# Optimization experiments

Measured on AMD Instinct MI355X. Metric: run time of the kernel, lower is better.

Reference implementation:

```python
import jax, jax.numpy as jnp
import numpy as np

NUM_LAYERS = 3
CHANNELS = 8
IN_CHANNELS = 8
MASK_OUT_STRIDE = 4


def resize_align_corners(x, oh, ow):
    # Bilinear resize with align_corners=True, x: [N, C, H, W]
    n, c, h, w = x.shape
    ys = jnp.linspace(0.0, h - 1.0, oh)
    xs = jnp.linspace(0.0, w - 1.0, ow)
    y0 = jnp.clip(jnp.floor(ys).astype(jnp.int32), 0, h - 2)
    x0 = jnp.clip(jnp.floor(xs).astype(jnp.int32), 0, w - 2)
    wy = (ys - y0.astype(ys.dtype)).astype(x.dtype)[None, None, :, None]
    wx = (xs - x0.astype(xs.dtype)).astype(x.dtype)[None, None, None, :]
    top = x[:, :, y0, :]
    bot = x[:, :, y0 + 1, :]
    row = top * (1.0 - wy) + bot * wy          # [n,c,oh,w]
    left = row[:, :, :, x0]
    right = row[:, :, :, x0 + 1]
    return left * (1.0 - wx) + right * wx       # [n,c,oh,ow]


def aligned_bilinear(t, factor):
    # Faithful port of adet.utils.comm.aligned_bilinear
    if factor == 1:
        return t
    h, w = t.shape[2], t.shape[3]
    t = jnp.pad(t, ((0, 0), (0, 0), (0, 1), (0, 1)), mode="edge")
    oh, ow = factor * h + 1, factor * w + 1
    t = resize_align_corners(t, oh, ow)
    p = factor // 2
    t = jnp.pad(t, ((0, 0), (0, 0), (p, 0), (p, 0)), mode="edge")
    return t[:, :, : oh - 1, : ow - 1]


def reference(mask_feats, mask_head_params, locations_inst, soi, im_inds, fpn_levels, mask_feat_stride):
    N, C, H, W = mask_feats.shape
    n_inst = mask_head_params.shape[0]
    # compute_locations at mask_feat_stride (x fastest, matching torch meshgrid order)
    half = mask_feat_stride // 2
    sx = jnp.arange(W, dtype=mask_feats.dtype) * mask_feat_stride + half
    sy = jnp.arange(H, dtype=mask_feats.dtype) * mask_feat_stride + half
    gy, gx = jnp.meshgrid(sy, sx, indexing="ij")
    locs = jnp.stack([gx.reshape(-1), gy.reshape(-1)], axis=1)  # [HW, 2]
    # relative coords, normalized by size-of-interest of instance's FPN level
    rel = locations_inst[:, None, :] - locs[None, :, :]          # [n, HW, 2]
    rel = jnp.transpose(rel, (0, 2, 1))                          # [n, 2, HW]
    rel = rel / soi[fpn_levels][:, None, None]
    feats = mask_feats[im_inds].reshape(n_inst, IN_CHANNELS, H * W)
    x = jnp.concatenate([rel.astype(mask_feats.dtype), feats], axis=1)  # [n, 10, HW]
    # parse_dynamic_params: split flat params into per-instance weights/biases
    wn = [(IN_CHANNELS + 2) * CHANNELS, CHANNELS * CHANNELS, CHANNELS * 1]
    bn = [CHANNELS, CHANNELS, 1]
    offs = np.cumsum([0] + wn + bn)
    parts = [mask_head_params[:, offs[i]:offs[i + 1]] for i in range(6)]
    w0 = parts[0].reshape(n_inst, CHANNELS, IN_CHANNELS + 2)
    w1 = parts[1].reshape(n_inst, CHANNELS, CHANNELS)
    w2 = parts[2].reshape(n_inst, 1, CHANNELS)
    b0, b1, b2 = parts[3], parts[4], parts[5]
    # per-instance dynamic MLP (1x1 grouped conv == batched matmul)
    x = jax.nn.relu(jnp.einsum("noi,nip->nop", w0, x) + b0[:, :, None])
    x = jax.nn.relu(jnp.einsum("noi,nip->nop", w1, x) + b1[:, :, None])
    x = jnp.einsum("noi,nip->nop", w2, x) + b2[:, :, None]
    logits = x.reshape(n_inst, 1, H, W)
    factor = int(mask_feat_stride // MASK_OUT_STRIDE)
    return aligned_bilinear(logits, factor)


def setup_inputs() -> dict:
    key = jax.random.key(0)
    k0, k1, k2, k3, k4 = jax.random.split(key, 5)
    N, C, H, W = 4, IN_CHANNELS, 128, 192
    n_inst = 128
    stride = 8
    num_gen_params = (IN_CHANNELS + 2) * CHANNELS + CHANNELS * CHANNELS + CHANNELS + CHANNELS + CHANNELS + 1  # 169
    mask_feats = jax.random.normal(k0, (N, C, H, W), dtype=jnp.float32)
    mask_head_params = jax.random.normal(k1, (n_inst, num_gen_params), dtype=jnp.float32) * 0.1
    locations_inst = jax.random.uniform(k2, (n_inst, 2), dtype=jnp.float32) * jnp.array([W * stride, H * stride], jnp.float32)
    soi = jnp.array([64.0, 128.0, 256.0, 512.0, 1024.0], jnp.float32)
    im_inds = jax.random.randint(k3, (n_inst,), 0, N)
    fpn_levels = jax.random.randint(k4, (n_inst,), 0, 5)
    return {
        "mask_feats": mask_feats,
        "mask_head_params": mask_head_params,
        "locations_inst": locations_inst,
        "soi": soi,
        "im_inds": im_inds,
        "fpn_levels": fpn_levels,
        "mask_feat_stride": stride,
    }
```

## Files before the change

### kernel.cpp

```cpp
#include <hip/hip_runtime.h>

#define HH 128
#define WW 192
#define HW (HH * WW)

typedef float f32x4 __attribute__((ext_vector_type(4)));
typedef __fp16 h2 __attribute__((ext_vector_type(2)));

__device__ __forceinline__ float relu(float v) { return fmaxf(v, 0.0f); }

__device__ __forceinline__ float fdot2(h2 a, h2 b, float c) {
#if __has_builtin(__builtin_amdgcn_fdot2)
    return __builtin_amdgcn_fdot2(a, b, c, false);
#else
    return fmaf((float)a.x, (float)b.x, fmaf((float)a.y, (float)b.y, c));
#endif
}
__device__ __forceinline__ h2 pkrtz(float a, float b) {
    return __builtin_amdgcn_cvt_pkrtz(a, b);
}


__global__ __launch_bounds__(512) void dmh_kernel(
    const float* __restrict__ mask_feats,
    const float* __restrict__ params,
    const float* __restrict__ locs,
    const float* __restrict__ soi,
    const int*   __restrict__ im_inds,
    const int*   __restrict__ fpn_levels,
    const int*   __restrict__ stride_p,
    float*       __restrict__ out)
{
    const int tid = threadIdx.x;
    const int c0 = blockIdx.x * 64;
    const int r0 = blockIdx.y * 32;
    const int n  = blockIdx.z;

    __shared__ h2    sWp[68];
    __shared__ float sF[33];
    __shared__ float tile[33 * 66];

    if (tid < 169) {
        float v = params[(size_t)n * 169 + tid];
        __fp16* sWh = reinterpret_cast<__fp16*>(sWp);
        if (tid < 80) {
            int o = tid / 10, k = tid - o * 10;
            if (k == 0)      sF[o] = v;
            else if (k == 1) sF[8 + o] = v;
            else { int f = k - 2; sWh[(o * 4 + (f >> 1)) * 2 + (f & 1)] = (__fp16)v; }
        } else if (tid < 144) {
            int t = tid - 80, o = t >> 3, i = t & 7;
            sWh[(32 + o * 4 + (i >> 1)) * 2 + (i & 1)] = (__fp16)v;
        } else if (tid < 152) {
            int o = tid - 144;
            sWh[(64 + (o >> 1)) * 2 + (o & 1)] = (__fp16)v;
        } else if (tid < 160) sF[16 + (tid - 152)] = v;
        else if (tid < 168)   sF[24 + (tid - 160)] = v;
        else                  sF[32] = v;
    }

    const int   stride = *stride_p;
    const float half_s = 0.5f * (float)stride;
    const float locx = locs[2 * n + 0];
    const float locy = locs[2 * n + 1];
    const float inv  = 1.0f / soi[fpn_levels[n]];
    const float* fb  = mask_feats + (size_t)im_inds[n] * 8 * HW;

    const int ir = tid >> 4;
    const int ic = (tid & 15) << 2;
    const int rr = r0 + ir, cc = c0 + ic;
    const float* fp = fb + rr * WW + cc;

    f32x4 xv[8];
    #pragma unroll
    for (int ch = 0; ch < 8; ++ch)
        xv[ch] = *reinterpret_cast<const f32x4*>(fp + ch * HW);

    __syncthreads();

    {
        const float rxd = -(float)stride * inv;
        float rx[4];
        rx[0] = (locx - (float)(cc * stride) - half_s) * inv;
        rx[1] = rx[0] + rxd; rx[2] = rx[1] + rxd; rx[3] = rx[2] + rxd;
        const float ry = (locy - (float)(rr * stride) - half_s) * inv;

        h2 xp[4][4];
        #pragma unroll
        for (int p = 0; p < 4; ++p)
            #pragma unroll
            for (int j = 0; j < 4; ++j)
                xp[p][j] = pkrtz(xv[2 * p][j], xv[2 * p + 1][j]);

        float h[8][4];
        #pragma unroll
        for (int o = 0; o < 8; ++o) {
            const h2 w0 = sWp[o * 4 + 0], w1 = sWp[o * 4 + 1],
                     w2 = sWp[o * 4 + 2], w3 = sWp[o * 4 + 3];
            float tO = fmaf(sF[8 + o], ry, sF[16 + o]);
            float wx = sF[o];
            #pragma unroll
            for (int j = 0; j < 4; ++j) {
                float acc = fmaf(wx, rx[j], tO);
                acc = fdot2(w0, xp[0][j], acc);
                acc = fdot2(w1, xp[1][j], acc);
                acc = fdot2(w2, xp[2][j], acc);
                acc = fdot2(w3, xp[3][j], acc);
                h[o][j] = acc;
            }
        }

        h2 hp[4][4];
        #pragma unroll
        for (int p = 0; p < 4; ++p)
            #pragma unroll
            for (int j = 0; j < 4; ++j)
                hp[p][j] = pkrtz(relu(h[2 * p][j]), relu(h[2 * p + 1][j]));

        float a[8][4];
        #pragma unroll
        for (int o = 0; o < 8; ++o) {
            const h2 w0 = sWp[32 + o * 4 + 0], w1 = sWp[32 + o * 4 + 1],
                     w2 = sWp[32 + o * 4 + 2], w3 = sWp[32 + o * 4 + 3];
            float b1 = sF[24 + o];
            #pragma unroll
            for (int j = 0; j < 4; ++j) {
                float acc = b1;
                acc = fdot2(w0, hp[0][j], acc);
                acc = fdot2(w1, hp[1][j], acc);
                acc = fdot2(w2, hp[2][j], acc);
                acc = fdot2(w3, hp[3][j], acc);
                a[o][j] = acc;
            }
        }

        const h2 v0 = sWp[64], v1 = sWp[65], v2 = sWp[66], v3 = sWp[67];
        const float b2v = sF[32];
        #pragma unroll
        for (int j = 0; j < 4; ++j) {
            h2 a0 = pkrtz(relu(a[0][j]), relu(a[1][j]));
            h2 a1 = pkrtz(relu(a[2][j]), relu(a[3][j]));
            h2 a2 = pkrtz(relu(a[4][j]), relu(a[5][j]));
            h2 a3 = pkrtz(relu(a[6][j]), relu(a[7][j]));
            float lg = b2v;
            lg = fdot2(v0, a0, lg);
            lg = fdot2(v1, a1, lg);
            lg = fdot2(v2, a2, lg);
            lg = fdot2(v3, a3, lg);
            tile[(ir + 1) * 66 + ic + 1 + j] = lg;
        }
    }

    if (tid < 97) {
        int r, c;
        if (tid < 65) { r = -1; c = tid - 1; }
        else          { r = tid - 65; c = -1; }
        int hr = min(max(r0 + r, 0), HH - 1);
        int hc = min(max(c0 + c, 0), WW - 1);
        const float* hfp = fb + hr * WW + hc;
        float rx  = (locx - (float)(hc * stride) - half_s) * inv;
        float ry2 = (locy - (float)(hr * stride) - half_s) * inv;
        h2 xp[4];
        #pragma unroll
        for (int p = 0; p < 4; ++p)
            xp[p] = pkrtz(hfp[(2 * p) * HW], hfp[(2 * p + 1) * HW]);
        float hh[8];
        #pragma unroll
        for (int o = 0; o < 8; ++o) {
            float acc = fmaf(sF[o], rx, fmaf(sF[8 + o], ry2, sF[16 + o]));
            #pragma unroll
            for (int p = 0; p < 4; ++p) acc = fdot2(sWp[o * 4 + p], xp[p], acc);
            hh[o] = acc;
        }
        h2 hp[4];
        #pragma unroll
        for (int p = 0; p < 4; ++p)
            hp[p] = pkrtz(relu(hh[2 * p]), relu(hh[2 * p + 1]));
        float aa[8];
        #pragma unroll
        for (int o = 0; o < 8; ++o) {
            float acc = sF[24 + o];
            #pragma unroll
            for (int p = 0; p < 4; ++p) acc = fdot2(sWp[32 + o * 4 + p], hp[p], acc);
            aa[o] = acc;
        }
        float lg = sF[32];
        #pragma unroll
        for (int p = 0; p < 4; ++p) {
            h2 ap = pkrtz(relu(aa[2 * p]), relu(aa[2 * p + 1]));
            lg = fdot2(sWp[64 + p], ap, lg);
        }
        tile[(r + 1) * 66 + (c + 1)] = lg;
    }
    __syncthreads();

    const int kx = tid & 31;
    const int ky = tid >> 5;
    float* ob = out + ((size_t)n * 256 + 2 * r0) * 384 + 2 * c0 + 4 * kx;
    #pragma unroll
    for (int yy = 0; yy < 4; ++yy) {
        int yt = ky * 4 + yy;
        int iy = yt - 1;
        int rbl = iy >> 1;
        int fy = iy & 1;
        float wy0 = fy ? 0.5f : 1.0f;
        float wy1 = fy ? 0.5f : 0.0f;
        int sr  = rbl + 1;
        int sr2 = sr + fy;
        const float* ra = &tile[sr  * 66 + 2 * kx];
        const float* rc = &tile[sr2 * 66 + 2 * kx];
        float t0 = fmaf(wy1, rc[0], wy0 * ra[0]);
        float t1 = fmaf(wy1, rc[1], wy0 * ra[1]);
        float t2 = fmaf(wy1, rc[2], wy0 * ra[2]);
        f32x4 o4;
        o4.x = 0.5f * (t0 + t1);
        o4.y = t1;
        o4.z = 0.5f * (t1 + t2);
        o4.w = t2;
        __builtin_nontemporal_store(o4, reinterpret_cast<f32x4*>(ob + (size_t)yt * 384));
    }
}

extern "C" void kernel_launch(void* const* d_in, const int* in_sizes, int n_in,
                              void* d_out, int out_size, void* d_ws, size_t ws_size,
                              hipStream_t stream) {
    const float* mask_feats = (const float*)d_in[0];
    const float* params     = (const float*)d_in[1];
    const float* locs       = (const float*)d_in[2];
    const float* soi        = (const float*)d_in[3];
    const int*   im_inds    = (const int*)d_in[4];
    const int*   fpn_levels = (const int*)d_in[5];
    const int*   stride_p   = (const int*)d_in[6];
    float* out = (float*)d_out;

    dim3 grid(WW / 64, HH / 32, 128);
    dim3 block(512);
    dmh_kernel<<<grid, block, 0, stream>>>(
        mask_feats, params, locs, soi, im_inds, fpn_levels, stride_p, out);
}
```

Measured before the change: 20.44 us.

## Map one wavefront per row pair and upsample in registers via lane shuffles

Each wavefront now owns two input rows across the full 192-column width, with each lane handling three columns. The next row's logits are recomputed locally, and horizontal neighbours come from a cross-lane shuffle instead of a shared-memory tile. This drops the LDS tile, the separate halo computation and the second barrier, and the bilinear upsample is done entirely in registers. The cost is about 50% recomputation of the MLP on the overlapping row, scalar three-element loads that are not 16-byte aligned, and narrower 8-byte stores.

After: 27.82 us. 36.1% more time.

```diff
diff --git a/kernel.cpp b/kernel.cpp
--- a/kernel.cpp
+++ b/kernel.cpp
@@ -4,24 +4,19 @@
 #define WW 192
 #define HW (HH * WW)
 
-typedef float f32x4 __attribute__((ext_vector_type(4)));
+typedef float f32x2v __attribute__((ext_vector_type(2)));
 typedef __fp16 h2 __attribute__((ext_vector_type(2)));
 
 __device__ __forceinline__ float relu(float v) { return fmaxf(v, 0.0f); }
-
 __device__ __forceinline__ float fdot2(h2 a, h2 b, float c) {
-#if __has_builtin(__builtin_amdgcn_fdot2)
     return __builtin_amdgcn_fdot2(a, b, c, false);
-#else
-    return fmaf((float)a.x, (float)b.x, fmaf((float)a.y, (float)b.y, c));
-#endif
 }
 __device__ __forceinline__ h2 pkrtz(float a, float b) {
     return __builtin_amdgcn_cvt_pkrtz(a, b);
 }
 
 
-__global__ __launch_bounds__(512) void dmh_kernel(
+__global__ __launch_bounds__(256) void dmh_kernel(
     const float* __restrict__ mask_feats,
     const float* __restrict__ params,
     const float* __restrict__ locs,
@@ -31,14 +26,15 @@
     const int*   __restrict__ stride_p,
     float*       __restrict__ out)
 {
-    const int tid = threadIdx.x;
-    const int c0 = blockIdx.x * 64;
-    const int r0 = blockIdx.y * 32;
-    const int n  = blockIdx.z;
+    const int tid  = threadIdx.x;
+    const int lane = tid & 63;
+    const int wid  = tid >> 6;
+    const int g    = blockIdx.x * 4 + wid;
+    const int r    = 2 * g;
+    const int n    = blockIdx.y;
 
     __shared__ h2    sWp[68];
     __shared__ float sF[33];
-    __shared__ float tile[33 * 66];
 
     if (tid < 169) {
         float v = params[(size_t)n * 169 + tid];
@@ -66,42 +62,46 @@
     const float inv  = 1.0f / soi[fpn_levels[n]];
     const float* fb  = mask_feats + (size_t)im_inds[n] * 8 * HW;
 
-    const int ir = tid >> 4;
-    const int ic = (tid & 15) << 2;
-    const int rr = r0 + ir, cc = c0 + ic;
-    const float* fp = fb + rr * WW + cc;
-
-    f32x4 xv[8];
+    __syncthreads();
+
+    const int col0 = 3 * lane;
+    const float rxd = -(float)stride * inv;
+    float rx0 = (locx - (float)(col0 * stride) - half_s) * inv;
+    float rx1 = rx0 + rxd;
+    float rx2 = rx1 + rxd;
+
+    float L[3][3];
     #pragma unroll
-    for (int ch = 0; ch < 8; ++ch)
-        xv[ch] = *reinterpret_cast<const f32x4*>(fp + ch * HW);
-
-    __syncthreads();
-
-    {
-        const float rxd = -(float)stride * inv;
-        float rx[4];
-        rx[0] = (locx - (float)(cc * stride) - half_s) * inv;
-        rx[1] = rx[0] + rxd; rx[2] = rx[1] + rxd; rx[3] = rx[2] + rxd;
-        const float ry = (locy - (float)(rr * stride) - half_s) * inv;
-
-        h2 xp[4][4];
+    for (int i = 0; i < 3; ++i) {
+        const int srow = min(r + i, HH - 1);
+        const float* fp = fb + srow * WW + col0;
+        const float ry = (locy - (float)(srow * stride) - half_s) * inv;
+
+        float x[8][3];
+        #pragma unroll
+        for (int ch = 0; ch < 8; ++ch) {
+            x[ch][0] = fp[ch * HW + 0];
+            x[ch][1] = fp[ch * HW + 1];
+            x[ch][2] = fp[ch * HW + 2];
+        }
+        h2 xp[4][3];
         #pragma unroll
         for (int p = 0; p < 4; ++p)
             #pragma unroll
-            for (int j = 0; j < 4; ++j)
-                xp[p][j] = pkrtz(xv[2 * p][j], xv[2 * p + 1][j]);
-
-        float h[8][4];
+            for (int j = 0; j < 3; ++j)
+                xp[p][j] = pkrtz(x[2 * p][j], x[2 * p + 1][j]);
+
+        float h[8][3];
         #pragma unroll
         for (int o = 0; o < 8; ++o) {
             const h2 w0 = sWp[o * 4 + 0], w1 = sWp[o * 4 + 1],
                      w2 = sWp[o * 4 + 2], w3 = sWp[o * 4 + 3];
             float tO = fmaf(sF[8 + o], ry, sF[16 + o]);
             float wx = sF[o];
-            #pragma unroll
-            for (int j = 0; j < 4; ++j) {
-                float acc = fmaf(wx, rx[j], tO);
+            float rxj[3] = {rx0, rx1, rx2};
+            #pragma unroll
+            for (int j = 0; j < 3; ++j) {
+                float acc = fmaf(wx, rxj[j], tO);
                 acc = fdot2(w0, xp[0][j], acc);
                 acc = fdot2(w1, xp[1][j], acc);
                 acc = fdot2(w2, xp[2][j], acc);
@@ -109,22 +109,21 @@
                 h[o][j] = acc;
             }
         }
-
-        h2 hp[4][4];
+        h2 hp[4][3];
         #pragma unroll
         for (int p = 0; p < 4; ++p)
             #pragma unroll
-            for (int j = 0; j < 4; ++j)
+            for (int j = 0; j < 3; ++j)
                 hp[p][j] = pkrtz(relu(h[2 * p][j]), relu(h[2 * p + 1][j]));
 
-        float a[8][4];
+        float a[8][3];
         #pragma unroll
         for (int o = 0; o < 8; ++o) {
             const h2 w0 = sWp[32 + o * 4 + 0], w1 = sWp[32 + o * 4 + 1],
                      w2 = sWp[32 + o * 4 + 2], w3 = sWp[32 + o * 4 + 3];
             float b1 = sF[24 + o];
             #pragma unroll
-            for (int j = 0; j < 4; ++j) {
+            for (int j = 0; j < 3; ++j) {
                 float acc = b1;
                 acc = fdot2(w0, hp[0][j], acc);
                 acc = fdot2(w1, hp[1][j], acc);
@@ -133,11 +132,10 @@
                 a[o][j] = acc;
             }
         }
-
         const h2 v0 = sWp[64], v1 = sWp[65], v2 = sWp[66], v3 = sWp[67];
         const float b2v = sF[32];
         #pragma unroll
-        for (int j = 0; j < 4; ++j) {
+        for (int j = 0; j < 3; ++j) {
             h2 a0 = pkrtz(relu(a[0][j]), relu(a[1][j]));
             h2 a1 = pkrtz(relu(a[2][j]), relu(a[3][j]));
             h2 a2 = pkrtz(relu(a[4][j]), relu(a[5][j]));
@@ -147,78 +145,42 @@
             lg = fdot2(v1, a1, lg);
             lg = fdot2(v2, a2, lg);
             lg = fdot2(v3, a3, lg);
-            tile[(ir + 1) * 66 + ic + 1 + j] = lg;
-        }
-    }
-
-    if (tid < 97) {
-        int r, c;
-        if (tid < 65) { r = -1; c = tid - 1; }
-        else          { r = tid - 65; c = -1; }
-        int hr = min(max(r0 + r, 0), HH - 1);
-        int hc = min(max(c0 + c, 0), WW - 1);
-        const float* hfp = fb + hr * WW + hc;
-        float rx  = (locx - (float)(hc * stride) - half_s) * inv;
-        float ry2 = (locy - (float)(hr * stride) - half_s) * inv;
-        h2 xp[4];
-        #pragma unroll
-        for (int p = 0; p < 4; ++p)
-            xp[p] = pkrtz(hfp[(2 * p) * HW], hfp[(2 * p + 1) * HW]);
-        float hh[8];
-        #pragma unroll
-        for (int o = 0; o < 8; ++o) {
-            float acc = fmaf(sF[o], rx, fmaf(sF[8 + o], ry2, sF[16 + o]));
-            #pragma unroll
-            for (int p = 0; p < 4; ++p) acc = fdot2(sWp[o * 4 + p], xp[p], acc);
-            hh[o] = acc;
-        }
-        h2 hp[4];
-        #pragma unroll
-        for (int p = 0; p < 4; ++p)
-            hp[p] = pkrtz(relu(hh[2 * p]), relu(hh[2 * p + 1]));
-        float aa[8];
-        #pragma unroll
-        for (int o = 0; o < 8; ++o) {
-            float acc = sF[24 + o];
-            #pragma unroll
-            for (int p = 0; p < 4; ++p) acc = fdot2(sWp[32 + o * 4 + p], hp[p], acc);
-            aa[o] = acc;
-        }
-        float lg = sF[32];
-        #pragma unroll
-        for (int p = 0; p < 4; ++p) {
-            h2 ap = pkrtz(relu(aa[2 * p]), relu(aa[2 * p + 1]));
-            lg = fdot2(sWp[64 + p], ap, lg);
-        }
-        tile[(r + 1) * 66 + (c + 1)] = lg;
-    }
-    __syncthreads();
-
-    const int kx = tid & 31;
-    const int ky = tid >> 5;
-    float* ob = out + ((size_t)n * 256 + 2 * r0) * 384 + 2 * c0 + 4 * kx;
+            L[i][j] = lg;
+        }
+    }
+
+    float ci[3][6];
     #pragma unroll
-    for (int yy = 0; yy < 4; ++yy) {
-        int yt = ky * 4 + yy;
-        int iy = yt - 1;
-        int rbl = iy >> 1;
-        int fy = iy & 1;
-        float wy0 = fy ? 0.5f : 1.0f;
-        float wy1 = fy ? 0.5f : 0.0f;
-        int sr  = rbl + 1;
-        int sr2 = sr + fy;
-        const float* ra = &tile[sr  * 66 + 2 * kx];
-        const float* rc = &tile[sr2 * 66 + 2 * kx];
-        float t0 = fmaf(wy1, rc[0], wy0 * ra[0]);
-        float t1 = fmaf(wy1, rc[1], wy0 * ra[1]);
-        float t2 = fmaf(wy1, rc[2], wy0 * ra[2]);
-        f32x4 o4;
-        o4.x = 0.5f * (t0 + t1);
-        o4.y = t1;
-        o4.z = 0.5f * (t1 + t2);
-        o4.w = t2;
-        __builtin_nontemporal_store(o4, reinterpret_cast<f32x4*>(ob + (size_t)yt * 384));
-    }
+    for (int i = 0; i < 3; ++i) {
+        float Lm1 = __shfl_up(L[i][2], 1);
+        if (lane == 0) Lm1 = L[i][0];
+        ci[i][0] = 0.5f * (Lm1 + L[i][0]);
+        ci[i][1] = L[i][0];
+        ci[i][2] = 0.5f * (L[i][0] + L[i][1]);
+        ci[i][3] = L[i][1];
+        ci[i][4] = 0.5f * (L[i][1] + L[i][2]);
+        ci[i][5] = L[i][2];
+    }
+
+    float* ob = out + (size_t)n * 256 * 384 + 6 * lane;
+    auto store_row = [&](int y, const float* v) {
+        float* p = ob + (size_t)y * 384;
+        f32x2v s0 = {v[0], v[1]}, s1 = {v[2], v[3]}, s2 = {v[4], v[5]};
+        *reinterpret_cast<f32x2v*>(p + 0) = s0;
+        *reinterpret_cast<f32x2v*>(p + 2) = s1;
+        *reinterpret_cast<f32x2v*>(p + 4) = s2;
+    };
+    float mid1[6], mid2[6];
+    #pragma unroll
+    for (int k = 0; k < 6; ++k) {
+        mid1[k] = 0.5f * (ci[0][k] + ci[1][k]);
+        mid2[k] = 0.5f * (ci[1][k] + ci[2][k]);
+    }
+    if (g == 0) store_row(0, ci[0]);
+    store_row(2 * r + 1, ci[0]);
+    store_row(2 * r + 2, mid1);
+    store_row(2 * r + 3, ci[1]);
+    if (2 * r + 4 <= 255) store_row(2 * r + 4, mid2);
 }
 
 extern "C" void kernel_launch(void* const* d_in, const int* in_sizes, int n_in,
@@ -233,8 +195,8 @@
     const int*   stride_p   = (const int*)d_in[6];
     float* out = (float*)d_out;
 
-    dim3 grid(WW / 64, HH / 32, 128);
-    dim3 block(512);
+    dim3 grid(16, 128);
+    dim3 block(256);
     dmh_kernel<<<grid, block, 0, stream>>>(
         mask_feats, params, locs, soi, im_inds, fpn_levels, stride_p, out);
 }
```

## Split fused kernel into logits pass and separate upsample pass via workspace

Applied to the files above, without the earlier changes.

Replaces the single fused kernel, which computed the MLP logits for a tile plus a recomputed halo and then upsampled from shared memory, with two kernels. The first writes full-resolution logits to a global workspace without halo recomputation. The second reads them back and does the 2x aligned bilinear upsample. This removes the redundant halo MLP work and the intra-block syncs, but adds a global round trip of the logits and a second launch.

Result: slower. 32.29 us (+58.0%).

```diff
diff --git a/kernel.cpp b/kernel.cpp
--- a/kernel.cpp
+++ b/kernel.cpp
@@ -3,25 +3,21 @@
 #define HH 128
 #define WW 192
 #define HW (HH * WW)
+#define PXI (HH * WW)
 
 typedef float f32x4 __attribute__((ext_vector_type(4)));
 typedef __fp16 h2 __attribute__((ext_vector_type(2)));
 
 __device__ __forceinline__ float relu(float v) { return fmaxf(v, 0.0f); }
-
 __device__ __forceinline__ float fdot2(h2 a, h2 b, float c) {
-#if __has_builtin(__builtin_amdgcn_fdot2)
     return __builtin_amdgcn_fdot2(a, b, c, false);
-#else
-    return fmaf((float)a.x, (float)b.x, fmaf((float)a.y, (float)b.y, c));
-#endif
 }
 __device__ __forceinline__ h2 pkrtz(float a, float b) {
     return __builtin_amdgcn_cvt_pkrtz(a, b);
 }
 
 
-__global__ __launch_bounds__(512) void dmh_kernel(
+__global__ __launch_bounds__(512) void logits_kernel(
     const float* __restrict__ mask_feats,
     const float* __restrict__ params,
     const float* __restrict__ locs,
@@ -29,16 +25,14 @@
     const int*   __restrict__ im_inds,
     const int*   __restrict__ fpn_levels,
     const int*   __restrict__ stride_p,
-    float*       __restrict__ out)
+    float*       __restrict__ ws)
 {
     const int tid = threadIdx.x;
-    const int c0 = blockIdx.x * 64;
-    const int r0 = blockIdx.y * 32;
-    const int n  = blockIdx.z;
+    const int bx  = blockIdx.x;
+    const int n   = blockIdx.y;
 
     __shared__ h2    sWp[68];
     __shared__ float sF[33];
-    __shared__ float tile[33 * 66];
 
     if (tid < 169) {
         float v = params[(size_t)n * 169 + tid];
@@ -66,10 +60,10 @@
     const float inv  = 1.0f / soi[fpn_levels[n]];
     const float* fb  = mask_feats + (size_t)im_inds[n] * 8 * HW;
 
-    const int ir = tid >> 4;
-    const int ic = (tid & 15) << 2;
-    const int rr = r0 + ir, cc = c0 + ic;
-    const float* fp = fb + rr * WW + cc;
+    const int px  = bx * 2048 + tid * 4;
+    const int row = px / WW;
+    const int col = px - row * WW;
+    const float* fp = fb + px;
 
     f32x4 xv[8];
     #pragma unroll
@@ -78,146 +72,117 @@
 
     __syncthreads();
 
-    {
-        const float rxd = -(float)stride * inv;
-        float rx[4];
-        rx[0] = (locx - (float)(cc * stride) - half_s) * inv;
-        rx[1] = rx[0] + rxd; rx[2] = rx[1] + rxd; rx[3] = rx[2] + rxd;
-        const float ry = (locy - (float)(rr * stride) - half_s) * inv;
-
-        h2 xp[4][4];
-        #pragma unroll
-        for (int p = 0; p < 4; ++p)
-            #pragma unroll
-            for (int j = 0; j < 4; ++j)
-                xp[p][j] = pkrtz(xv[2 * p][j], xv[2 * p + 1][j]);
-
-        float h[8][4];
-        #pragma unroll
-        for (int o = 0; o < 8; ++o) {
-            const h2 w0 = sWp[o * 4 + 0], w1 = sWp[o * 4 + 1],
-                     w2 = sWp[o * 4 + 2], w3 = sWp[o * 4 + 3];
-            float tO = fmaf(sF[8 + o], ry, sF[16 + o]);
-            float wx = sF[o];
-            #pragma unroll
-            for (int j = 0; j < 4; ++j) {
-                float acc = fmaf(wx, rx[j], tO);
-                acc = fdot2(w0, xp[0][j], acc);
-                acc = fdot2(w1, xp[1][j], acc);
-                acc = fdot2(w2, xp[2][j], acc);
-                acc = fdot2(w3, xp[3][j], acc);
-                h[o][j] = acc;
-            }
+    const float rxd = -(float)stride * inv;
+    float rx[4];
+    rx[0] = (locx - (float)(col * stride) - half_s) * inv;
+    rx[1] = rx[0] + rxd; rx[2] = rx[1] + rxd; rx[3] = rx[2] + rxd;
+    const float ry = (locy - (float)(row * stride) - half_s) * inv;
+
+    h2 xp[4][4];
+    #pragma unroll
+    for (int p = 0; p < 4; ++p)
+        #pragma unroll
+        for (int j = 0; j < 4; ++j)
+            xp[p][j] = pkrtz(xv[2 * p][j], xv[2 * p + 1][j]);
+
+    float h[8][4];
+    #pragma unroll
+    for (int o = 0; o < 8; ++o) {
+        const h2 w0 = sWp[o * 4 + 0], w1 = sWp[o * 4 + 1],
+                 w2 = sWp[o * 4 + 2], w3 = sWp[o * 4 + 3];
+        float tO = fmaf(sF[8 + o], ry, sF[16 + o]);
+        float wx = sF[o];
+        #pragma unroll
+        for (int j = 0; j < 4; ++j) {
+            float acc = fmaf(wx, rx[j], tO);
+            acc = fdot2(w0, xp[0][j], acc);
+            acc = fdot2(w1, xp[1][j], acc);
+            acc = fdot2(w2, xp[2][j], acc);
+            acc = fdot2(w3, xp[3][j], acc);
+            h[o][j] = acc;
         }
-
-        h2 hp[4][4];
-        #pragma unroll
-        for (int p = 0; p < 4; ++p)
-            #pragma unroll
-            for (int j = 0; j < 4; ++j)
-                hp[p][j] = pkrtz(relu(h[2 * p][j]), relu(h[2 * p + 1][j]));
-
-        float a[8][4];
-        #pragma unroll
-        for (int o = 0; o < 8; ++o) {
-            const h2 w0 = sWp[32 + o * 4 + 0], w1 = sWp[32 + o * 4 + 1],
-                     w2 = sWp[32 + o * 4 + 2], w3 = sWp[32 + o * 4 + 3];
-            float b1 = sF[24 + o];
-            #pragma unroll
-            for (int j = 0; j < 4; ++j) {
-                float acc = b1;
-                acc = fdot2(w0, hp[0][j], acc);
-                acc = fdot2(w1, hp[1][j], acc);
-                acc = fdot2(w2, hp[2][j], acc);
-                acc = fdot2(w3, hp[3][j], acc);
-                a[o][j] = acc;
-            }
+    }
+    h2 hp[4][4];
+    #pragma unroll
+    for (int p = 0; p < 4; ++p)
+        #pragma unroll
+        for (int j = 0; j < 4; ++j)
+            hp[p][j] = pkrtz(relu(h[2 * p][j]), relu(h[2 * p + 1][j]));
+
+    float a[8][4];
+    #pragma unroll
+    for (int o = 0; o < 8; ++o) {
+        const h2 w0 = sWp[32 + o * 4 + 0], w1 = sWp[32 + o * 4 + 1],
+                 w2 = sWp[32 + o * 4 + 2], w3 = sWp[32 + o * 4 + 3];
+        float b1 = sF[24 + o];
+        #pragma unroll
+        for (int j = 0; j < 4; ++j) {
+            float acc = b1;
+            acc = fdot2(w0, hp[0][j], acc);
+            acc = fdot2(w1, hp[1][j], acc);
+            acc = fdot2(w2, hp[2][j], acc);
+            acc = fdot2(w3, hp[3][j], acc);
+            a[o][j] = acc;
         }
-
-        const h2 v0 = sWp[64], v1 = sWp[65], v2 = sWp[66], v3 = sWp[67];
-        const float b2v = sF[32];
-        #pragma unroll
-        for (int j = 0; j < 4; ++j) {
-            h2 a0 = pkrtz(relu(a[0][j]), relu(a[1][j]));
-            h2 a1 = pkrtz(relu(a[2][j]), relu(a[3][j]));
-            h2 a2 = pkrtz(relu(a[4][j]), relu(a[5][j]));
-            h2 a3 = pkrtz(relu(a[6][j]), relu(a[7][j]));
-            float lg = b2v;
-            lg = fdot2(v0, a0, lg);
-            lg = fdot2(v1, a1, lg);
-            lg = fdot2(v2, a2, lg);
-            lg = fdot2(v3, a3, lg);
-            tile[(ir + 1) * 66 + ic + 1 + j] = lg;
-        }
-    }
-
-    if (tid < 97) {
-        int r, c;
-        if (tid < 65) { r = -1; c = tid - 1; }
-        else          { r = tid - 65; c = -1; }
-        int hr = min(max(r0 + r, 0), HH - 1);
-        int hc = min(max(c0 + c, 0), WW - 1);
-        const float* hfp = fb + hr * WW + hc;
-        float rx  = (locx - (float)(hc * stride) - half_s) * inv;
-        float ry2 = (locy - (float)(hr * stride) - half_s) * inv;
-        h2 xp[4];
-        #pragma unroll
-        for (int p = 0; p < 4; ++p)
-            xp[p] = pkrtz(hfp[(2 * p) * HW], hfp[(2 * p + 1) * HW]);
-        float hh[8];
-        #pragma unroll
-        for (int o = 0; o < 8; ++o) {
-            float acc = fmaf(sF[o], rx, fmaf(sF[8 + o], ry2, sF[16 + o]));
-            #pragma unroll
-            for (int p = 0; p < 4; ++p) acc = fdot2(sWp[o * 4 + p], xp[p], acc);
-            hh[o] = acc;
-        }
-        h2 hp[4];
-        #pragma unroll
-        for (int p = 0; p < 4; ++p)
-            hp[p] = pkrtz(relu(hh[2 * p]), relu(hh[2 * p + 1]));
-        float aa[8];
-        #pragma unroll
-        for (int o = 0; o < 8; ++o) {
-            float acc = sF[24 + o];
-            #pragma unroll
-            for (int p = 0; p < 4; ++p) acc = fdot2(sWp[32 + o * 4 + p], hp[p], acc);
-            aa[o] = acc;
-        }
-        float lg = sF[32];
-        #pragma unroll
-        for (int p = 0; p < 4; ++p) {
-            h2 ap = pkrtz(relu(aa[2 * p]), relu(aa[2 * p + 1]));
-            lg = fdot2(sWp[64 + p], ap, lg);
-        }
-        tile[(r + 1) * 66 + (c + 1)] = lg;
-    }
-    __syncthreads();
-
-    const int kx = tid & 31;
-    const int ky = tid >> 5;
-    float* ob = out + ((size_t)n * 256 + 2 * r0) * 384 + 2 * c0 + 4 * kx;
-    #pragma unroll
-    for (int yy = 0; yy < 4; ++yy) {
-        int yt = ky * 4 + yy;
-        int iy = yt - 1;
-        int rbl = iy >> 1;
-        int fy = iy & 1;
-        float wy0 = fy ? 0.5f : 1.0f;
-        float wy1 = fy ? 0.5f : 0.0f;
-        int sr  = rbl + 1;
-        int sr2 = sr + fy;
-        const float* ra = &tile[sr  * 66 + 2 * kx];
-        const float* rc = &tile[sr2 * 66 + 2 * kx];
-        float t0 = fmaf(wy1, rc[0], wy0 * ra[0]);
-        float t1 = fmaf(wy1, rc[1], wy0 * ra[1]);
-        float t2 = fmaf(wy1, rc[2], wy0 * ra[2]);
+    }
+    const h2 v0 = sWp[64], v1 = sWp[65], v2 = sWp[66], v3 = sWp[67];
+    const float b2v = sF[32];
+    f32x4 lg;
+    #pragma unroll
+    for (int j = 0; j < 4; ++j) {
+        h2 a0 = pkrtz(relu(a[0][j]), relu(a[1][j]));
+        h2 a1 = pkrtz(relu(a[2][j]), relu(a[3][j]));
+        h2 a2 = pkrtz(relu(a[4][j]), relu(a[5][j]));
+        h2 a3 = pkrtz(relu(a[6][j]), relu(a[7][j]));
+        float l = b2v;
+        l = fdot2(v0, a0, l);
+        l = fdot2(v1, a1, l);
+        l = fdot2(v2, a2, l);
+        l = fdot2(v3, a3, l);
+        lg[j] = l;
+    }
+    *reinterpret_cast<f32x4*>(ws + (size_t)n * PXI + px) = lg;
+}
+
+__global__ __launch_bounds__(256) void upsample_kernel(
+    const float* __restrict__ ws,
+    float*       __restrict__ out)
+{
+    const int tid = threadIdx.x;
+    const int g0  = blockIdx.x * 1024 + tid;
+
+    #pragma unroll
+    for (int k = 0; k < 4; ++k) {
+        const int g   = g0 + k * 256;
+        const int yg  = g / 96;
+        const int f4c = g - yg * 96;
+        const int n   = yg >> 8;
+        const int y   = yg & 255;
+
+        const int iy = y - 1;
+        const int rb = iy >> 1;
+        const int fy = iy & 1;
+        const float wy0 = fy ? 0.5f : 1.0f;
+        const float wy1 = fy ? 0.5f : 0.0f;
+        const int r1 = max(rb, 0);
+        const int r2 = rb + fy;
+
+        const float* La = ws + (size_t)n * PXI + r1 * WW;
+        const float* Lb = ws + (size_t)n * PXI + r2 * WW;
+
+        const int m0 = 2 * f4c - 1;
+        const int mc = max(m0, 0);
+        float t0 = fmaf(wy1, Lb[mc],     wy0 * La[mc]);
+        float t1 = fmaf(wy1, Lb[m0 + 1], wy0 * La[m0 + 1]);
+        float t2 = fmaf(wy1, Lb[m0 + 2], wy0 * La[m0 + 2]);
+
         f32x4 o4;
         o4.x = 0.5f * (t0 + t1);
         o4.y = t1;
         o4.z = 0.5f * (t1 + t2);
         o4.w = t2;
-        __builtin_nontemporal_store(o4, reinterpret_cast<f32x4*>(ob + (size_t)yt * 384));
+        __builtin_nontemporal_store(o4,
+            reinterpret_cast<f32x4*>(out + (size_t)yg * 384 + 4 * f4c));
     }
 }
 
@@ -232,9 +197,11 @@
     const int*   fpn_levels = (const int*)d_in[5];
     const int*   stride_p   = (const int*)d_in[6];
     float* out = (float*)d_out;
-
-    dim3 grid(WW / 64, HH / 32, 128);
-    dim3 block(512);
-    dmh_kernel<<<grid, block, 0, stream>>>(
-        mask_feats, params, locs, soi, im_inds, fpn_levels, stride_p, out);
-}
+    float* ws  = (float*)d_ws;
+
+    dim3 gridA(12, 128);
+    logits_kernel<<<gridA, dim3(512), 0, stream>>>(
+        mask_feats, params, locs, soi, im_inds, fpn_levels, stride_p, ws);
+
+    upsample_kernel<<<dim3(3072), dim3(256), 0, stream>>>(ws, out);
+}
```
